# Kernel tuning notes

Measured on AMD Instinct MI355X. Metric: run time of the kernel, lower is better.

Reference implementation:

```python
import jax, jax.numpy as jnp
import numpy as np

ND, NP_, B = 20000, 10000, 4096
DE, PE = 320000, 160000
FEAT = 300 + 1024 + 1024 + 1024  # 3372


def leaky(x):
    return jnp.where(x > 0, x, 0.01 * x)


def gcn_conv(x, W, b, edge_index, edge_weight, n):
    # PyG GCNConv (eval): x' = D^-1/2 (A + I) D^-1/2 (x W) + b, with edge weights
    h = x @ W  # [n, out]
    row, col = edge_index[0], edge_index[1]
    loop = jnp.arange(n)
    row = jnp.concatenate([row, loop])
    col = jnp.concatenate([col, loop])
    ew = jnp.concatenate([edge_weight, jnp.ones((n,), edge_weight.dtype)])
    deg = jax.ops.segment_sum(ew, col, num_segments=n)
    dinv = jnp.where(deg > 0, jax.lax.rsqrt(deg), 0.0)
    norm = dinv[row] * ew * dinv[col]  # [E+n]
    out = jax.ops.segment_sum(h[row] * norm[:, None], col, num_segments=n)
    return out + b


def _lin_init(k, fi, fo):
    return jax.random.normal(k, (fi, fo), jnp.float32) * (1.0 / np.sqrt(fi))


def setup_inputs():
    key = jax.random.key(0)
    ks = jax.random.split(key, 32)
    inp = {}
    inp['d_index'] = jax.random.randint(ks[0], (B,), 0, ND)
    inp['p_index'] = jax.random.randint(ks[1], (B,), 0, NP_)
    inp['d_vecs'] = jax.random.normal(ks[2], (B, 300), jnp.float32)
    inp['p_embeddings'] = jax.random.normal(ks[3], (B, 1024), jnp.float32)
    inp['d_ecfps'] = jax.random.normal(ks[4], (ND, 1024), jnp.float32)
    inp['d_edge_index'] = jax.random.randint(ks[5], (2, DE), 0, ND)
    inp['d_edge_weight'] = jax.random.uniform(ks[6], (DE,), jnp.float32)
    inp['p_gos'] = jax.random.normal(ks[7], (NP_, 2812), jnp.float32)
    inp['p_edge_index'] = jax.random.randint(ks[8], (2, PE), 0, NP_)
    inp['p_edge_weight'] = jax.random.uniform(ks[9], (PE,), jnp.float32)
    # parameters
    inp['d_gcn_W'] = _lin_init(ks[10], 1024, 1024); inp['d_gcn_b'] = jnp.zeros((1024,), jnp.float32)
    inp['p_gcn_W'] = _lin_init(ks[11], 2812, 1024); inp['p_gcn_b'] = jnp.zeros((1024,), jnp.float32)
    inp['enc_W1'] = _lin_init(ks[12], FEAT, 1024); inp['enc_b1'] = jnp.zeros((1024,), jnp.float32)
    inp['enc_W2'] = _lin_init(ks[13], 1024, 256); inp['enc_b2'] = jnp.zeros((256,), jnp.float32)
    inp['dec_W1'] = _lin_init(ks[14], 256, 1024); inp['dec_b1'] = jnp.zeros((1024,), jnp.float32)
    inp['dec_W2'] = _lin_init(ks[15], 1024, FEAT); inp['dec_b2'] = jnp.zeros((FEAT,), jnp.float32)
    inp['out_W1'] = _lin_init(ks[16], 256, 128); inp['out_b1'] = jnp.zeros((128,), jnp.float32)
    inp['bn_gamma'] = jnp.ones((128,), jnp.float32)
    inp['bn_beta'] = jnp.zeros((128,), jnp.float32)
    inp['bn_mean'] = jnp.zeros((128,), jnp.float32)
    inp['bn_var'] = jnp.ones((128,), jnp.float32)
    inp['out_W2'] = _lin_init(ks[17], 128, 1); inp['out_b2'] = jnp.zeros((1,), jnp.float32)
    return inp


def reference(d_index, p_index, d_vecs, p_embeddings, d_ecfps, d_edge_index,
              d_edge_weight, p_gos, p_edge_index, p_edge_weight,
              d_gcn_W, d_gcn_b, p_gcn_W, p_gcn_b,
              enc_W1, enc_b1, enc_W2, enc_b2,
              dec_W1, dec_b1, dec_W2, dec_b2,
              out_W1, out_b1, bn_gamma, bn_beta, bn_mean, bn_var, out_W2, out_b2):
    # GCN branches (Dropout is identity in eval mode)
    ecfps = leaky(gcn_conv(d_ecfps, d_gcn_W, d_gcn_b, d_edge_index, d_edge_weight, ND))[d_index]
    gos = leaky(gcn_conv(p_gos, p_gcn_W, p_gcn_b, p_edge_index, p_edge_weight, NP_))[p_index]
    feature = jnp.concatenate([d_vecs, p_embeddings, ecfps, gos], axis=1)  # [B, 3372]
    encoded = leaky(leaky(feature @ enc_W1 + enc_b1) @ enc_W2 + enc_b2)  # [B, 256]
    decoded = leaky(leaky(encoded @ dec_W1 + dec_b1) @ dec_W2 + dec_b2)  # [B, 3372]
    h = encoded @ out_W1 + out_b1
    h = (h - bn_mean) * jax.lax.rsqrt(bn_var + 1e-5) * bn_gamma + bn_beta  # BN (eval)
    y = leaky(h) @ out_W2 + out_b2  # [B, 1]
    return (y, encoded, decoded, feature)
```

## Files before the change

### kernel.cpp

```cpp
#include <hip/hip_runtime.h>

#define ND    20000
#define NPn   10000
#define Bsz   4096
#define DE    320000
#define PEe   160000
#define FEAT  3372

#define ENC_OFF  4096ull
#define DEC_OFF  1052672ull
#define FEAT_OFF 14864384ull

typedef unsigned short u16;
typedef unsigned int   u32;
typedef __bf16 bf16x8 __attribute__((ext_vector_type(8)));
typedef float  f32x4  __attribute__((ext_vector_type(4)));

__device__ __forceinline__ float bf2f(u16 u) {
    u32 v = ((u32)u) << 16;
    return __builtin_bit_cast(float, v);
}
__device__ __forceinline__ u16 f2bf(float f) {
    u32 x = __builtin_bit_cast(u32, f);
    x += 0x7fffu + ((x >> 16) & 1u);
    return (u16)(x >> 16);
}
__device__ __forceinline__ float lrelu(float x) { return x > 0.f ? x : 0.01f * x; }

__device__ __forceinline__ float ldv(const void* p, size_t i, int f32) {
    return f32 ? ((const float*)p)[i] : bf2f(((const u16*)p)[i]);
}
__device__ __forceinline__ void stv(void* p, size_t i, int f32, float v) {
    if (f32) ((float*)p)[i] = v; else ((u16*)p)[i] = f2bf(v);
}

typedef __attribute__((address_space(1))) const void GASV;
typedef __attribute__((address_space(3))) void LASV;
__device__ __forceinline__ void gld16(const u16* g, u16* l) {
    __builtin_amdgcn_global_load_lds((GASV*)g, (LASV*)l, 16, 0, 0);
}

__global__ void detect_dtype(const u32* __restrict__ ew, int* __restrict__ flag)
{
    int t = threadIdx.x, bad = 0;
    for (int i = t; i < 256; i += 64)
        if ((ew[i] & 0xffffu) > 0x4200u) bad = 1;
    unsigned long long m = __ballot(bad);
    if (t == 0) *flag = (m != 0ull) ? 1 : 0;
}

__global__ __launch_bounds__(256) void transpose_split(const void* __restrict__ W,
                                                       u16* __restrict__ Th,
                                                       u16* __restrict__ Tl,
                                                       int K, int N, int Kp,
                                                       const int* __restrict__ flagp)
{
    const int f32 = *flagp;
    __shared__ float tile[32][33];
    const int k0 = blockIdx.x * 32, n0 = blockIdx.y * 32;
    const int tx = threadIdx.x & 31, ty = threadIdx.x >> 5;
    for (int i = 0; i < 4; ++i) {
        int k = k0 + ty + 8 * i, n = n0 + tx;
        float v = 0.f;
        if (k < K && n < N) v = ldv(W, (size_t)k * N + n, f32);
        tile[ty + 8 * i][tx] = v;
    }
    __syncthreads();
    for (int i = 0; i < 4; ++i) {
        int n = n0 + ty + 8 * i, k = k0 + tx;
        if (n < N && k < Kp) {
            float v = tile[tx][ty + 8 * i];
            u16 h = f2bf(v);
            Th[(size_t)n * Kp + k] = h;
            Tl[(size_t)n * Kp + k] = f2bf(v - bf2f(h));
        }
    }
}

__global__ void deg_accum(const int* __restrict__ ei, const void* __restrict__ ew,
                          float* __restrict__ deg, int E, const int* __restrict__ flagp)
{
    const int f32 = *flagp;
    int e = blockIdx.x * blockDim.x + threadIdx.x;
    if (e >= E) return;
    atomicAdd(&deg[ei[E + e]], ldv(ew, e, f32));
}

__global__ void dinv_kernel(float* __restrict__ deg, int n)
{
    int i = blockIdx.x * blockDim.x + threadIdx.x;
    if (i >= n) return;
    deg[i] = rsqrtf(deg[i] + 1.0f);
}

__global__ void csr_count(const int* __restrict__ ei, int* __restrict__ cnt, int E)
{
    int e = blockIdx.x * blockDim.x + threadIdx.x;
    if (e >= E) return;
    atomicAdd(&cnt[ei[E + e]], 1);
}

__global__ __launch_bounds__(256) void scan_kernel(const int* __restrict__ cnt,
                                                   int* __restrict__ offs,
                                                   int* __restrict__ cur, int n)
{
    __shared__ int tot[256];
    __shared__ int pref[257];
    const int t = threadIdx.x;
    const int chunk = (n + 255) / 256;
    const int s0 = t * chunk;
    const int s1 = (s0 + chunk < n) ? (s0 + chunk) : n;
    int s = 0;
    for (int i = s0; i < s1; ++i) s += cnt[i];
    tot[t] = s;
    __syncthreads();
    if (t == 0) {
        int run = 0;
        for (int i = 0; i < 256; ++i) { pref[i] = run; run += tot[i]; }
        pref[256] = run;
    }
    __syncthreads();
    int run = pref[t];
    for (int i = s0; i < s1; ++i) { offs[i] = run; cur[i] = run; run += cnt[i]; }
    if (t == 255) offs[n] = pref[256];
}

__global__ void csr_fill(const int* __restrict__ ei, const void* __restrict__ ew,
                         int* __restrict__ cur, int* __restrict__ crow,
                         float* __restrict__ cw, int E, const int* __restrict__ flagp)
{
    const int f32 = *flagp;
    int e = blockIdx.x * blockDim.x + threadIdx.x;
    if (e >= E) return;
    int c = ei[E + e];
    int p = atomicAdd(&cur[c], 1);
    crow[p] = ei[e];
    cw[p]   = ldv(ew, e, f32);
}

__global__ __launch_bounds__(256) void aggregate(const void* __restrict__ X, int ldx,
                                                 int ncols,
                                                 const int* __restrict__ bidx,
                                                 const float* __restrict__ dinv,
                                                 const int* __restrict__ offs,
                                                 const int* __restrict__ crow,
                                                 const float* __restrict__ cw,
                                                 const int* __restrict__ flagp,
                                                 u16* __restrict__ outH,
                                                 u16* __restrict__ outL, int ldo)
{
    const int f32 = *flagp;
    const int b = blockIdx.x, t = threadIdx.x;
    const int node = bidx[b];
    const int nch = ncols >> 2;
    const float dc = dinv[node];
    float acc[3][4];
#pragma unroll
    for (int i = 0; i < 3; ++i)
        for (int j = 0; j < 4; ++j) acc[i][j] = 0.f;

    {
        const float sw = dc * dc;
        const size_t rb = (size_t)node * ldx;
#pragma unroll
        for (int i = 0; i < 3; ++i) {
            int c = t + 256 * i;
            if (c < nch) {
                float v[4];
                if (f32) {
                    float4 x = *(const float4*)((const float*)X + rb + 4 * c);
                    v[0] = x.x; v[1] = x.y; v[2] = x.z; v[3] = x.w;
                } else {
                    uint2 x = *(const uint2*)((const u16*)X + rb + 4 * c);
                    v[0] = bf2f((u16)(x.x & 0xffffu)); v[1] = bf2f((u16)(x.x >> 16));
                    v[2] = bf2f((u16)(x.y & 0xffffu)); v[3] = bf2f((u16)(x.y >> 16));
                }
                for (int j = 0; j < 4; ++j) acc[i][j] += v[j] * sw;
            }
        }
    }
    const int e1 = offs[node + 1];
    for (int e = offs[node]; e < e1; ++e) {
        const int r = crow[e];
        const float nrm = dinv[r] * cw[e] * dc;
        const size_t rb = (size_t)r * ldx;
#pragma unroll
        for (int i = 0; i < 3; ++i) {
            int c = t + 256 * i;
            if (c < nch) {
                float v[4];
                if (f32) {
                    float4 x = *(const float4*)((const float*)X + rb + 4 * c);
                    v[0] = x.x; v[1] = x.y; v[2] = x.z; v[3] = x.w;
                } else {
                    uint2 x = *(const uint2*)((const u16*)X + rb + 4 * c);
                    v[0] = bf2f((u16)(x.x & 0xffffu)); v[1] = bf2f((u16)(x.x >> 16));
                    v[2] = bf2f((u16)(x.y & 0xffffu)); v[3] = bf2f((u16)(x.y >> 16));
                }
                for (int j = 0; j < 4; ++j) acc[i][j] += v[j] * nrm;
            }
        }
    }
    const size_t ob = (size_t)b * ldo;
#pragma unroll
    for (int i = 0; i < 3; ++i) {
        int c = t + 256 * i;
        if (c < nch) {
            u16 h[4], l[4];
#pragma unroll
            for (int j = 0; j < 4; ++j) {
                h[j] = f2bf(acc[i][j]);
                l[j] = f2bf(acc[i][j] - bf2f(h[j]));
            }
            uint2 hv, lv;
            hv.x = (u32)h[0] | ((u32)h[1] << 16); hv.y = (u32)h[2] | ((u32)h[3] << 16);
            lv.x = (u32)l[0] | ((u32)l[1] << 16); lv.y = (u32)l[2] | ((u32)l[3] << 16);
            *(uint2*)(outH + ob + 4 * c) = hv;
            *(uint2*)(outL + ob + 4 * c) = lv;
        }
    }
    if (t == 0)
        for (int j = ncols; j < ldo; ++j) { outH[ob + j] = 0; outL[ob + j] = 0; }
}

__global__ __launch_bounds__(512, 2) void gemm_planes(
        const u16* __restrict__ Ah, const u16* __restrict__ Al, int lda,
        const u16* __restrict__ Bh, const u16* __restrict__ Bl, int ldb,
        void* __restrict__ C, int cmode, unsigned long long c_off, int ldc,
        u16* __restrict__ Ch, u16* __restrict__ Cl, int ldcp,
        const void* __restrict__ bias, int M, int N, int Kp,
        int do_leaky, const int* __restrict__ flagp)
{
    const int flag = *flagp;
    const int cf32 = cmode ? flag : 1;
    __shared__ u16 smAh[2][128 * 32], smAl[2][128 * 32];
    __shared__ u16 smBh[2][128 * 32], smBl[2][128 * 32];
    const int tid = threadIdx.x;
    const int m0 = blockIdx.y * 128, n0 = blockIdx.x * 128;
    const int w = tid >> 6, lane = tid & 63;
    const int wy = w >> 1, wx = w & 1, lr = lane & 15, q = lane >> 4;
    f32x4 acc[2][4] = {};

    const int sr = tid >> 2;
    const int sc = (tid & 3) * 8;
    const size_t gA = (size_t)(m0 + sr) * lda + sc;
    const size_t gB = (size_t)(n0 + sr) * ldb + sc;
    const int wb = w << 9;

    auto stage = [&](int k0, int buf) {
        gld16(Ah + gA + k0, &smAh[buf][wb]);
        gld16(Al + gA + k0, &smAl[buf][wb]);
        gld16(Bh + gB + k0, &smBh[buf][wb]);
        gld16(Bl + gB + k0, &smBl[buf][wb]);
    };

    stage(0, 0);
    __syncthreads();
    int cur = 0;
    for (int k0 = 0; k0 < Kp; k0 += 32) {
        const int nxt = k0 + 32;
        if (nxt < Kp) stage(nxt, cur ^ 1);
        bf16x8 bh[4], bl[4];
#pragma unroll
        for (int ni = 0; ni < 4; ++ni) {
            bh[ni] = *(const bf16x8*)&smBh[cur][(wx * 64 + ni * 16 + lr) * 32 + q * 8];
            bl[ni] = *(const bf16x8*)&smBl[cur][(wx * 64 + ni * 16 + lr) * 32 + q * 8];
        }
#pragma unroll
        for (int mi = 0; mi < 2; ++mi) {
            bf16x8 ah = *(const bf16x8*)&smAh[cur][(wy * 32 + mi * 16 + lr) * 32 + q * 8];
            bf16x8 al = *(const bf16x8*)&smAl[cur][(wy * 32 + mi * 16 + lr) * 32 + q * 8];
#pragma unroll
            for (int ni = 0; ni < 4; ++ni) {
                acc[mi][ni] = __builtin_amdgcn_mfma_f32_16x16x32_bf16(ah, bh[ni], acc[mi][ni], 0, 0, 0);
                acc[mi][ni] = __builtin_amdgcn_mfma_f32_16x16x32_bf16(ah, bl[ni], acc[mi][ni], 0, 0, 0);
                acc[mi][ni] = __builtin_amdgcn_mfma_f32_16x16x32_bf16(al, bh[ni], acc[mi][ni], 0, 0, 0);
            }
        }
        __syncthreads();
        cur ^= 1;
    }

#pragma unroll
    for (int mi = 0; mi < 2; ++mi)
#pragma unroll
        for (int r = 0; r < 4; ++r) {
            const int gm = m0 + wy * 32 + mi * 16 + q * 4 + r;
#pragma unroll
            for (int ni = 0; ni < 4; ++ni) {
                const int gn = n0 + wx * 64 + ni * 16 + lr;
                if (gn >= N) continue;
                float v = acc[mi][ni][r];
                if (bias) v += ldv(bias, gn, flag);
                if (do_leaky) v = lrelu(v);
                float vq = v;
                if (C) {
                    const size_t ci = (size_t)c_off + (size_t)gm * ldc + gn;
                    if (cf32) ((float*)C)[ci] = v;
                    else { u16 hh = f2bf(v); ((u16*)C)[ci] = hh; vq = bf2f(hh); }
                }
                if (Ch) {
                    const size_t pi = (size_t)gm * ldcp + gn;
                    u16 h = f2bf(vq);
                    Ch[pi] = h;
                    Cl[pi] = f2bf(vq - bf2f(h));
                }
            }
        }
}

__global__ __launch_bounds__(256) void concat(const void* __restrict__ d_vecs,
                                              const void* __restrict__ p_emb,
                                              void* __restrict__ out,
                                              u16* __restrict__ Fh,
                                              u16* __restrict__ Fl,
                                              const int* __restrict__ flagp)
{
    const int f32 = *flagp;
    const int b = blockIdx.x;
    const size_t fb = FEAT_OFF + (size_t)b * FEAT;
    const size_t pb = (size_t)b * 3392;
    for (int j = threadIdx.x; j < 1324; j += 256) {
        float v = (j < 300) ? ldv(d_vecs, (size_t)b * 300 + j, f32)
                            : ldv(p_emb, (size_t)b * 1024 + (j - 300), f32);
        stv(out, fb + j, f32, v);
        float vq = f32 ? v : bf2f(f2bf(v));
        u16 h = f2bf(vq);
        Fh[pb + j] = h;
        Fl[pb + j] = f2bf(vq - bf2f(h));
    }
    for (int j = 3372 + threadIdx.x; j < 3392; j += 256) {
        Fh[pb + j] = 0; Fl[pb + j] = 0;
    }
}

__global__ __launch_bounds__(128) void head(void* __restrict__ out,
                                            const void* __restrict__ W1,
                                            const void* __restrict__ b1,
                                            const void* __restrict__ g,
                                            const void* __restrict__ be,
                                            const void* __restrict__ mu,
                                            const void* __restrict__ vr,
                                            const void* __restrict__ W2,
                                            const void* __restrict__ b2,
                                            const int* __restrict__ flagp)
{
    const int f32 = *flagp;
    __shared__ float se[256];
    __shared__ float red[128];
    const int b = blockIdx.x, t = threadIdx.x;
    const size_t eb = ENC_OFF + (size_t)b * 256;
    se[t]       = ldv(out, eb + t, f32);
    se[t + 128] = ldv(out, eb + 128 + t, f32);
    __syncthreads();
    float acc = 0.f;
    for (int k = 0; k < 256; ++k) acc += se[k] * ldv(W1, (size_t)k * 128 + t, f32);
    acc += ldv(b1, t, f32);
    float bn = (acc - ldv(mu, t, f32)) * rsqrtf(ldv(vr, t, f32) + 1e-5f) * ldv(g, t, f32)
             + ldv(be, t, f32);
    red[t] = lrelu(bn) * ldv(W2, t, f32);
    __syncthreads();
    for (int s = 64; s > 0; s >>= 1) {
        if (t < s) red[t] += red[t + s];
        __syncthreads();
    }
    if (t == 0) stv(out, (size_t)b, f32, red[0] + ldv(b2, 0, f32));
}

extern "C" void kernel_launch(void* const* d_in, const int* in_sizes, int n_in,
                              void* d_out, int out_size, void* d_ws, size_t ws_size,
                              hipStream_t stream)
{
    (void)in_sizes; (void)n_in; (void)out_size; (void)ws_size;

    const int*  d_index = (const int*)d_in[0];
    const int*  p_index = (const int*)d_in[1];
    const void* d_vecs  = d_in[2];
    const void* p_emb   = d_in[3];
    const void* d_ecfps = d_in[4];
    const int*  d_ei    = (const int*)d_in[5];
    const void* d_ew    = d_in[6];
    const void* p_gos   = d_in[7];
    const int*  p_ei    = (const int*)d_in[8];
    const void* p_ew    = d_in[9];
    const void* d_gcn_W = d_in[10];
    const void* d_gcn_b = d_in[11];
    const void* p_gcn_W = d_in[12];
    const void* p_gcn_b = d_in[13];
    const void* enc_W1  = d_in[14];
    const void* enc_b1  = d_in[15];
    const void* enc_W2  = d_in[16];
    const void* enc_b2  = d_in[17];
    const void* dec_W1  = d_in[18];
    const void* dec_b1  = d_in[19];
    const void* dec_W2  = d_in[20];
    const void* dec_b2  = d_in[21];
    const void* out_W1  = d_in[22];
    const void* out_b1  = d_in[23];
    const void* bn_g    = d_in[24];
    const void* bn_b    = d_in[25];
    const void* bn_m    = d_in[26];
    const void* bn_v    = d_in[27];
    const void* out_W2  = d_in[28];
    const void* out_b2  = d_in[29];

    char* base = (char*)d_ws;
    size_t off = 0;
    auto alloc = [&](size_t bytes) -> void* {
        void* p = base + off;
        off = (off + bytes + 255) & ~(size_t)255;
        return p;
    };
    u16* Th_d  = (u16*)alloc((size_t)1024 * 1024 * 2);
    u16* Tl_d  = (u16*)alloc((size_t)1024 * 1024 * 2);
    u16* Th_p  = (u16*)alloc((size_t)1024 * 2816 * 2);
    u16* Tl_p  = (u16*)alloc((size_t)1024 * 2816 * 2);
    u16* Th_e1 = (u16*)alloc((size_t)1024 * 3392 * 2);
    u16* Tl_e1 = (u16*)alloc((size_t)1024 * 3392 * 2);
    u16* Th_e2 = (u16*)alloc((size_t)256  * 1024 * 2);
    u16* Tl_e2 = (u16*)alloc((size_t)256  * 1024 * 2);
    u16* Th_d1 = (u16*)alloc((size_t)1024 * 256  * 2);
    u16* Tl_d1 = (u16*)alloc((size_t)1024 * 256  * 2);
    u16* Th_d2 = (u16*)alloc((size_t)3456 * 1024 * 2);
    u16* Tl_d2 = (u16*)alloc((size_t)3456 * 1024 * 2);
    u16* AgDh = (u16*)alloc((size_t)Bsz * 1024 * 2);
    u16* AgDl = (u16*)alloc((size_t)Bsz * 1024 * 2);
    u16* AgPh = (u16*)alloc((size_t)Bsz * 2816 * 2);
    u16* AgPl = (u16*)alloc((size_t)Bsz * 2816 * 2);
    u16* Fh   = (u16*)alloc((size_t)Bsz * 3392 * 2);
    u16* Fl   = (u16*)alloc((size_t)Bsz * 3392 * 2);
    u16* E1h = AgDh;
    u16* E1l = AgDl;
    u16* Eh  = AgPh;
    u16* El  = AgPh + (size_t)Bsz * 256;
    u16* D1h = AgPl;
    u16* D1l = AgPl + (size_t)Bsz * 1024;
    float* deg_d  = (float*)alloc((size_t)ND  * 4);
    float* deg_p  = (float*)alloc((size_t)NPn * 4);
    int*   cnt_d  = (int*)alloc((size_t)ND * 4);
    int*   offs_d = (int*)alloc((size_t)(ND + 1) * 4);
    int*   cur_d  = (int*)alloc((size_t)ND * 4);
    int*   cnt_p  = (int*)alloc((size_t)NPn * 4);
    int*   offs_p = (int*)alloc((size_t)(NPn + 1) * 4);
    int*   cur_p  = (int*)alloc((size_t)NPn * 4);
    int*   crow_d = (int*)alloc((size_t)DE * 4);
    float* cw_d   = (float*)alloc((size_t)DE * 4);
    int*   crow_p = (int*)alloc((size_t)PEe * 4);
    float* cw_p   = (float*)alloc((size_t)PEe * 4);
    int*   flagp  = (int*)alloc(16);

    detect_dtype<<<1, 64, 0, stream>>>((const u32*)d_ew, flagp);
    hipMemsetAsync(deg_d, 0, (size_t)ND * 4, stream);
    hipMemsetAsync(deg_p, 0, (size_t)NPn * 4, stream);
    hipMemsetAsync(cnt_d, 0, (size_t)ND * 4, stream);
    hipMemsetAsync(cnt_p, 0, (size_t)NPn * 4, stream);

    transpose_split<<<dim3(32, 32),  256, 0, stream>>>(d_gcn_W, Th_d,  Tl_d,  1024, 1024, 1024, flagp);
    transpose_split<<<dim3(88, 32),  256, 0, stream>>>(p_gcn_W, Th_p,  Tl_p,  2812, 1024, 2816, flagp);
    transpose_split<<<dim3(106, 32), 256, 0, stream>>>(enc_W1,  Th_e1, Tl_e1, 3372, 1024, 3392, flagp);
    transpose_split<<<dim3(32, 8),   256, 0, stream>>>(enc_W2,  Th_e2, Tl_e2, 1024, 256,  1024, flagp);
    transpose_split<<<dim3(8, 32),   256, 0, stream>>>(dec_W1,  Th_d1, Tl_d1, 256,  1024, 256,  flagp);
    transpose_split<<<dim3(32, 106), 256, 0, stream>>>(dec_W2,  Th_d2, Tl_d2, 1024, 3372, 1024, flagp);

    deg_accum<<<(DE + 255) / 256, 256, 0, stream>>>(d_ei, d_ew, deg_d, DE, flagp);
    deg_accum<<<(PEe + 255) / 256, 256, 0, stream>>>(p_ei, p_ew, deg_p, PEe, flagp);
    dinv_kernel<<<(ND + 255) / 256, 256, 0, stream>>>(deg_d, ND);
    dinv_kernel<<<(NPn + 255) / 256, 256, 0, stream>>>(deg_p, NPn);
    csr_count<<<(DE + 255) / 256, 256, 0, stream>>>(d_ei, cnt_d, DE);
    csr_count<<<(PEe + 255) / 256, 256, 0, stream>>>(p_ei, cnt_p, PEe);
    scan_kernel<<<1, 256, 0, stream>>>(cnt_d, offs_d, cur_d, ND);
    scan_kernel<<<1, 256, 0, stream>>>(cnt_p, offs_p, cur_p, NPn);
    csr_fill<<<(DE + 255) / 256, 256, 0, stream>>>(d_ei, d_ew, cur_d, crow_d, cw_d, DE, flagp);
    csr_fill<<<(PEe + 255) / 256, 256, 0, stream>>>(p_ei, p_ew, cur_p, crow_p, cw_p, PEe, flagp);

    aggregate<<<Bsz, 256, 0, stream>>>(d_ecfps, 1024, 1024, d_index, deg_d,
                                       offs_d, crow_d, cw_d, flagp, AgDh, AgDl, 1024);
    aggregate<<<Bsz, 256, 0, stream>>>(p_gos, 2812, 2812, p_index, deg_p,
                                       offs_p, crow_p, cw_p, flagp, AgPh, AgPl, 2816);

    gemm_planes<<<dim3(8, 32), 512, 0, stream>>>(AgDh, AgDl, 1024, Th_d, Tl_d, 1024,
                                                 d_out, 1, FEAT_OFF + 1324, FEAT,
                                                 Fh + 1324, Fl + 1324, 3392,
                                                 d_gcn_b, Bsz, 1024, 1024, 1, flagp);
    gemm_planes<<<dim3(8, 32), 512, 0, stream>>>(AgPh, AgPl, 2816, Th_p, Tl_p, 2816,
                                                 d_out, 1, FEAT_OFF + 2348, FEAT,
                                                 Fh + 2348, Fl + 2348, 3392,
                                                 p_gcn_b, Bsz, 1024, 2816, 1, flagp);

    concat<<<Bsz, 256, 0, stream>>>(d_vecs, p_emb, d_out, Fh, Fl, flagp);

    gemm_planes<<<dim3(8, 32), 512, 0, stream>>>(Fh, Fl, 3392, Th_e1, Tl_e1, 3392,
                                                 nullptr, 0, 0, 0,
                                                 E1h, E1l, 1024,
                                                 enc_b1, Bsz, 1024, 3392, 1, flagp);
    gemm_planes<<<dim3(2, 32), 512, 0, stream>>>(E1h, E1l, 1024, Th_e2, Tl_e2, 1024,
                                                 d_out, 1, ENC_OFF, 256,
                                                 Eh, El, 256,
                                                 enc_b2, Bsz, 256, 1024, 1, flagp);
    gemm_planes<<<dim3(8, 32), 512, 0, stream>>>(Eh, El, 256, Th_d1, Tl_d1, 256,
                                                 nullptr, 0, 0, 0,
                                                 D1h, D1l, 1024,
                                                 dec_b1, Bsz, 1024, 256, 1, flagp);
    gemm_planes<<<dim3(27, 32), 512, 0, stream>>>(D1h, D1l, 1024, Th_d2, Tl_d2, 1024,
                                                  d_out, 1, DEC_OFF, FEAT,
                                                  nullptr, nullptr, 0,
                                                  dec_b2, Bsz, 3372, 1024, 1, flagp);

    head<<<Bsz, 128, 0, stream>>>(d_out, out_W1, out_b1, bn_g, bn_b,
                                  bn_m, bn_v, out_W2, out_b2, flagp);
}
```

Before: 1.229 ms.

## Add split-K GEMM with combine kernel, drop low-plane MFMA for bf16 inputs

Adds split-K to the plane GEMM: blocks along z each compute a K chunk and write fp32 partials, and a new combine kernel sums them and applies bias, leaky ReLU and the output/plane writes. Each GEMM launch has only 256 tiles, so this is meant to give more parallelism on a many-CU GPU. It also drops the shared-memory double buffer so more blocks fit per CU (launch bounds now 6), and skips the B low-plane load and MFMA when inputs are bf16. The costs are extra partial-buffer traffic, an extra launch per GEMM, and no overlap of loads with compute.

```diff
diff --git a/kernel.cpp b/kernel.cpp
--- a/kernel.cpp
+++ b/kernel.cpp
@@ -13,6 +13,7 @@
 
 typedef unsigned short u16;
 typedef unsigned int   u32;
+typedef unsigned long long u64;
 typedef __bf16 bf16x8 __attribute__((ext_vector_type(8)));
 typedef float  f32x4  __attribute__((ext_vector_type(4)));
 
@@ -223,90 +224,157 @@
         for (int j = ncols; j < ldo; ++j) { outH[ob + j] = 0; outL[ob + j] = 0; }
 }
 
-__global__ __launch_bounds__(512, 2) void gemm_planes(
+__global__ __launch_bounds__(512, 6) void gemm_planes(
         const u16* __restrict__ Ah, const u16* __restrict__ Al, int lda,
         const u16* __restrict__ Bh, const u16* __restrict__ Bl, int ldb,
-        void* __restrict__ C, int cmode, unsigned long long c_off, int ldc,
+        void* __restrict__ C, int cmode, u64 c_off, int ldc,
         u16* __restrict__ Ch, u16* __restrict__ Cl, int ldcp,
         const void* __restrict__ bias, int M, int N, int Kp,
-        int do_leaky, const int* __restrict__ flagp)
+        int do_leaky, const int* __restrict__ flagp,
+        int kChunk, float* __restrict__ Part)
 {
     const int flag = *flagp;
-    const int cf32 = cmode ? flag : 1;
-    __shared__ u16 smAh[2][128 * 32], smAl[2][128 * 32];
-    __shared__ u16 smBh[2][128 * 32], smBl[2][128 * 32];
+    __shared__ u16 smAh[4096], smAl[4096], smBh[4096], smBl[4096];
     const int tid = threadIdx.x;
     const int m0 = blockIdx.y * 128, n0 = blockIdx.x * 128;
     const int w = tid >> 6, lane = tid & 63;
     const int wy = w >> 1, wx = w & 1, lr = lane & 15, q = lane >> 4;
     f32x4 acc[2][4] = {};
 
-    const int sr = tid >> 2;
-    const int sc = (tid & 3) * 8;
+    const int sr = tid >> 2, sc = (tid & 3) * 8;
     const size_t gA = (size_t)(m0 + sr) * lda + sc;
     const size_t gB = (size_t)(n0 + sr) * ldb + sc;
     const int wb = w << 9;
 
-    auto stage = [&](int k0, int buf) {
-        gld16(Ah + gA + k0, &smAh[buf][wb]);
-        gld16(Al + gA + k0, &smAl[buf][wb]);
-        gld16(Bh + gB + k0, &smBh[buf][wb]);
-        gld16(Bl + gB + k0, &smBl[buf][wb]);
-    };
-
-    stage(0, 0);
-    __syncthreads();
-    int cur = 0;
-    for (int k0 = 0; k0 < Kp; k0 += 32) {
-        const int nxt = k0 + 32;
-        if (nxt < Kp) stage(nxt, cur ^ 1);
-        bf16x8 bh[4], bl[4];
-#pragma unroll
-        for (int ni = 0; ni < 4; ++ni) {
-            bh[ni] = *(const bf16x8*)&smBh[cur][(wx * 64 + ni * 16 + lr) * 32 + q * 8];
-            bl[ni] = *(const bf16x8*)&smBl[cur][(wx * 64 + ni * 16 + lr) * 32 + q * 8];
-        }
-#pragma unroll
-        for (int mi = 0; mi < 2; ++mi) {
-            bf16x8 ah = *(const bf16x8*)&smAh[cur][(wy * 32 + mi * 16 + lr) * 32 + q * 8];
-            bf16x8 al = *(const bf16x8*)&smAl[cur][(wy * 32 + mi * 16 + lr) * 32 + q * 8];
+    const int kBeg = Part ? blockIdx.z * kChunk : 0;
+    int kEnd = Part ? kBeg + kChunk : Kp;
+    if (kEnd > Kp) kEnd = Kp;
+
+    for (int k0 = kBeg; k0 < kEnd; k0 += 32) {
+        gld16(Ah + gA + k0, &smAh[wb]);
+        gld16(Al + gA + k0, &smAl[wb]);
+        gld16(Bh + gB + k0, &smBh[wb]);
+        if (flag) gld16(Bl + gB + k0, &smBl[wb]);
+        __syncthreads();
+        if (flag) {
+            bf16x8 bh[4], bl[4];
 #pragma unroll
             for (int ni = 0; ni < 4; ++ni) {
-                acc[mi][ni] = __builtin_amdgcn_mfma_f32_16x16x32_bf16(ah, bh[ni], acc[mi][ni], 0, 0, 0);
-                acc[mi][ni] = __builtin_amdgcn_mfma_f32_16x16x32_bf16(ah, bl[ni], acc[mi][ni], 0, 0, 0);
-                acc[mi][ni] = __builtin_amdgcn_mfma_f32_16x16x32_bf16(al, bh[ni], acc[mi][ni], 0, 0, 0);
+                bh[ni] = *(const bf16x8*)&smBh[(wx * 64 + ni * 16 + lr) * 32 + q * 8];
+                bl[ni] = *(const bf16x8*)&smBl[(wx * 64 + ni * 16 + lr) * 32 + q * 8];
+            }
+#pragma unroll
+            for (int mi = 0; mi < 2; ++mi) {
+                bf16x8 ah = *(const bf16x8*)&smAh[(wy * 32 + mi * 16 + lr) * 32 + q * 8];
+                bf16x8 al = *(const bf16x8*)&smAl[(wy * 32 + mi * 16 + lr) * 32 + q * 8];
+#pragma unroll
+                for (int ni = 0; ni < 4; ++ni) {
+                    acc[mi][ni] = __builtin_amdgcn_mfma_f32_16x16x32_bf16(ah, bh[ni], acc[mi][ni], 0, 0, 0);
+                    acc[mi][ni] = __builtin_amdgcn_mfma_f32_16x16x32_bf16(al, bh[ni], acc[mi][ni], 0, 0, 0);
+                    acc[mi][ni] = __builtin_amdgcn_mfma_f32_16x16x32_bf16(ah, bl[ni], acc[mi][ni], 0, 0, 0);
+                }
+            }
+        } else {
+            bf16x8 bh[4];
+#pragma unroll
+            for (int ni = 0; ni < 4; ++ni)
+                bh[ni] = *(const bf16x8*)&smBh[(wx * 64 + ni * 16 + lr) * 32 + q * 8];
+#pragma unroll
+            for (int mi = 0; mi < 2; ++mi) {
+                bf16x8 ah = *(const bf16x8*)&smAh[(wy * 32 + mi * 16 + lr) * 32 + q * 8];
+                bf16x8 al = *(const bf16x8*)&smAl[(wy * 32 + mi * 16 + lr) * 32 + q * 8];
+#pragma unroll
+                for (int ni = 0; ni < 4; ++ni) {
+                    acc[mi][ni] = __builtin_amdgcn_mfma_f32_16x16x32_bf16(ah, bh[ni], acc[mi][ni], 0, 0, 0);
+                    acc[mi][ni] = __builtin_amdgcn_mfma_f32_16x16x32_bf16(al, bh[ni], acc[mi][ni], 0, 0, 0);
+                }
             }
         }
         __syncthreads();
-        cur ^= 1;
-    }
-
-#pragma unroll
-    for (int mi = 0; mi < 2; ++mi)
-#pragma unroll
-        for (int r = 0; r < 4; ++r) {
-            const int gm = m0 + wy * 32 + mi * 16 + q * 4 + r;
-#pragma unroll
-            for (int ni = 0; ni < 4; ++ni) {
-                const int gn = n0 + wx * 64 + ni * 16 + lr;
-                if (gn >= N) continue;
-                float v = acc[mi][ni][r];
-                if (bias) v += ldv(bias, gn, flag);
-                if (do_leaky) v = lrelu(v);
-                float vq = v;
-                if (C) {
-                    const size_t ci = (size_t)c_off + (size_t)gm * ldc + gn;
-                    if (cf32) ((float*)C)[ci] = v;
-                    else { u16 hh = f2bf(v); ((u16*)C)[ci] = hh; vq = bf2f(hh); }
+    }
+
+    if (Part) {
+        float* P = Part + (size_t)blockIdx.z * ((size_t)M * N);
+#pragma unroll
+        for (int mi = 0; mi < 2; ++mi)
+#pragma unroll
+            for (int r = 0; r < 4; ++r) {
+                const int gm = m0 + wy * 32 + mi * 16 + q * 4 + r;
+                float* row = P + (size_t)gm * N + n0 + wx * 64 + lr;
+#pragma unroll
+                for (int ni = 0; ni < 4; ++ni)
+                    row[ni * 16] = acc[mi][ni][r];
+            }
+    } else {
+#pragma unroll
+        for (int mi = 0; mi < 2; ++mi)
+#pragma unroll
+            for (int r = 0; r < 4; ++r) {
+                const int gm = m0 + wy * 32 + mi * 16 + q * 4 + r;
+                if (gm >= M) continue;
+#pragma unroll
+                for (int ni = 0; ni < 4; ++ni) {
+                    const int gn = n0 + wx * 64 + ni * 16 + lr;
+                    if (gn >= N) continue;
+                    float v = acc[mi][ni][r];
+                    if (bias) v += ldv(bias, gn, flag);
+                    if (do_leaky) v = lrelu(v);
+                    float vq = v;
+                    if (C) {
+                        const size_t ci = (size_t)c_off + (size_t)gm * ldc + gn;
+                        const int cf32 = cmode ? flag : 1;
+                        if (cf32) ((float*)C)[ci] = v;
+                        else { u16 hh = f2bf(v); ((u16*)C)[ci] = hh; vq = bf2f(hh); }
+                    }
+                    if (Ch) {
+                        const size_t pi = (size_t)gm * ldcp + gn;
+                        u16 h = f2bf(vq);
+                        Ch[pi] = h;
+                        Cl[pi] = f2bf(vq - bf2f(h));
+                    }
                 }
-                if (Ch) {
-                    const size_t pi = (size_t)gm * ldcp + gn;
-                    u16 h = f2bf(vq);
-                    Ch[pi] = h;
-                    Cl[pi] = f2bf(vq - bf2f(h));
-                }
-            }
-        }
+            }
+    }
+}
+
+__global__ __launch_bounds__(256) void combine_split(
+        const float* __restrict__ Part, int S, int M, int N,
+        void* __restrict__ C, int cmode, u64 c_off, int ldc,
+        u16* __restrict__ Ch, u16* __restrict__ Cl, int ldcp,
+        const void* __restrict__ bias, int do_leaky,
+        const int* __restrict__ flagp)
+{
+    const int flag = *flagp;
+    const int cf32 = cmode ? flag : 1;
+    const size_t MN = (size_t)M * N;
+    size_t g = ((size_t)blockIdx.x * 256 + threadIdx.x) * 4;
+    if (g >= MN) return;
+    float4 v = *(const float4*)(Part + g);
+    for (int s = 1; s < S; ++s) {
+        float4 u = *(const float4*)(Part + (size_t)s * MN + g);
+        v.x += u.x; v.y += u.y; v.z += u.z; v.w += u.w;
+    }
+    const int gm = (int)(g / N), gn0 = (int)(g - (size_t)gm * N);
+    float e[4] = {v.x, v.y, v.z, v.w};
+#pragma unroll
+    for (int i = 0; i < 4; ++i) {
+        const int gn = gn0 + i;
+        float val = e[i];
+        if (bias) val += ldv(bias, gn, flag);
+        if (do_leaky) val = lrelu(val);
+        float vq = val;
+        if (C) {
+            const size_t ci = (size_t)c_off + (size_t)gm * ldc + gn;
+            if (cf32) ((float*)C)[ci] = val;
+            else { u16 hh = f2bf(val); ((u16*)C)[ci] = hh; vq = bf2f(hh); }
+        }
+        if (Ch) {
+            const size_t pi = (size_t)gm * ldcp + gn;
+            u16 h = f2bf(vq);
+            Ch[pi] = h;
+            Cl[pi] = f2bf(vq - bf2f(h));
+        }
+    }
 }
 
 __global__ __launch_bounds__(256) void concat(const void* __restrict__ d_vecs,
@@ -371,7 +439,7 @@
                               void* d_out, int out_size, void* d_ws, size_t ws_size,
                               hipStream_t stream)
 {
-    (void)in_sizes; (void)n_in; (void)out_size; (void)ws_size;
+    (void)in_sizes; (void)n_in; (void)out_size;
 
     const int*  d_index = (const int*)d_in[0];
     const int*  p_index = (const int*)d_in[1];
@@ -448,6 +516,15 @@
     int*   crow_p = (int*)alloc((size_t)PEe * 4);
     float* cw_p   = (float*)alloc((size_t)PEe * 4);
     int*   flagp  = (int*)alloc(16);
+    const size_t need4 = (size_t)4 * Bsz * 1024 * 4;
+    const size_t need2 = (size_t)2 * Bsz * 1024 * 4;
+    float* Part = nullptr;
+    int Sbig = 1, Se2 = 1, Sd1 = 1;
+    if (off + need4 + 512 <= ws_size) {
+        Part = (float*)alloc(need4); Sbig = 4; Se2 = 8; Sd1 = 2;
+    } else if (off + need2 + 512 <= ws_size) {
+        Part = (float*)alloc(need2); Sbig = 2; Se2 = 8; Sd1 = 2;
+    }
 
     detect_dtype<<<1, 64, 0, stream>>>((const u32*)d_ew, flagp);
     hipMemsetAsync(deg_d, 0, (size_t)ND * 4, stream);
@@ -478,33 +555,50 @@
     aggregate<<<Bsz, 256, 0, stream>>>(p_gos, 2812, 2812, p_index, deg_p,
                                        offs_p, crow_p, cw_p, flagp, AgPh, AgPl, 2816);
 
-    gemm_planes<<<dim3(8, 32), 512, 0, stream>>>(AgDh, AgDl, 1024, Th_d, Tl_d, 1024,
-                                                 d_out, 1, FEAT_OFF + 1324, FEAT,
-                                                 Fh + 1324, Fl + 1324, 3392,
-                                                 d_gcn_b, Bsz, 1024, 1024, 1, flagp);
-    gemm_planes<<<dim3(8, 32), 512, 0, stream>>>(AgPh, AgPl, 2816, Th_p, Tl_p, 2816,
-                                                 d_out, 1, FEAT_OFF + 2348, FEAT,
-                                                 Fh + 2348, Fl + 2348, 3392,
-                                                 p_gcn_b, Bsz, 1024, 2816, 1, flagp);
+    auto G = [&](const u16* Ah_, const u16* Al_, int lda_,
+                 const u16* Bh_, const u16* Bl_, int ldb_,
+                 void* C_, int cmode_, u64 coff_, int ldc_,
+                 u16* Ch_, u16* Cl_, int ldcp_,
+                 const void* bias_, int N_, int Kp_, int S_) {
+        const int nx = (N_ + 127) / 128;
+        if (S_ > 1 && Part) {
+            const int kc = ((Kp_ / S_ + 31) / 32) * 32;
+            gemm_planes<<<dim3(nx, 32, S_), 512, 0, stream>>>(
+                Ah_, Al_, lda_, Bh_, Bl_, ldb_,
+                nullptr, 0, 0, 0, nullptr, nullptr, 0,
+                nullptr, Bsz, N_, Kp_, 0, flagp, kc, Part);
+            combine_split<<<(Bsz * N_) / 1024, 256, 0, stream>>>(
+                Part, S_, Bsz, N_,
+                C_, cmode_, coff_, ldc_, Ch_, Cl_, ldcp_, bias_, 1, flagp);
+        } else {
+            gemm_planes<<<dim3(nx, 32, 1), 512, 0, stream>>>(
+                Ah_, Al_, lda_, Bh_, Bl_, ldb_,
+                C_, cmode_, coff_, ldc_, Ch_, Cl_, ldcp_,
+                bias_, Bsz, N_, Kp_, 1, flagp, 0, nullptr);
+        }
+    };
+
+    G(AgDh, AgDl, 1024, Th_d, Tl_d, 1024,
+      d_out, 1, FEAT_OFF + 1324, FEAT, Fh + 1324, Fl + 1324, 3392,
+      d_gcn_b, 1024, 1024, Sbig);
+    G(AgPh, AgPl, 2816, Th_p, Tl_p, 2816,
+      d_out, 1, FEAT_OFF + 2348, FEAT, Fh + 2348, Fl + 2348, 3392,
+      p_gcn_b, 1024, 2816, Sbig);
 
     concat<<<Bsz, 256, 0, stream>>>(d_vecs, p_emb, d_out, Fh, Fl, flagp);
 
-    gemm_planes<<<dim3(8, 32), 512, 0, stream>>>(Fh, Fl, 3392, Th_e1, Tl_e1, 3392,
-                                                 nullptr, 0, 0, 0,
-                                                 E1h, E1l, 1024,
-                                                 enc_b1, Bsz, 1024, 3392, 1, flagp);
-    gemm_planes<<<dim3(2, 32), 512, 0, stream>>>(E1h, E1l, 1024, Th_e2, Tl_e2, 1024,
-                                                 d_out, 1, ENC_OFF, 256,
-                                                 Eh, El, 256,
-                                                 enc_b2, Bsz, 256, 1024, 1, flagp);
-    gemm_planes<<<dim3(8, 32), 512, 0, stream>>>(Eh, El, 256, Th_d1, Tl_d1, 256,
-                                                 nullptr, 0, 0, 0,
-                                                 D1h, D1l, 1024,
-                                                 dec_b1, Bsz, 1024, 256, 1, flagp);
-    gemm_planes<<<dim3(27, 32), 512, 0, stream>>>(D1h, D1l, 1024, Th_d2, Tl_d2, 1024,
-                                                  d_out, 1, DEC_OFF, FEAT,
-                                                  nullptr, nullptr, 0,
-                                                  dec_b2, Bsz, 3372, 1024, 1, flagp);
+    G(Fh, Fl, 3392, Th_e1, Tl_e1, 3392,
+      nullptr, 0, 0, 0, E1h, E1l, 1024,
+      enc_b1, 1024, 3392, Sbig);
+    G(E1h, E1l, 1024, Th_e2, Tl_e2, 1024,
+      d_out, 1, ENC_OFF, 256, Eh, El, 256,
+      enc_b2, 256, 1024, Se2);
+    G(Eh, El, 256, Th_d1, Tl_d1, 256,
+      nullptr, 0, 0, 0, D1h, D1l, 1024,
+      dec_b1, 1024, 256, Sd1);
+    G(D1h, D1l, 1024, Th_d2, Tl_d2, 1024,
+      d_out, 1, DEC_OFF, FEAT, nullptr, nullptr, 0,
+      dec_b2, 3372, 1024, 1);
 
     head<<<Bsz, 128, 0, stream>>>(d_out, out_W1, out_b1, bn_g, bn_b,
                                   bn_m, bn_v, out_W2, out_b2, flagp);
```

Measured after the change: 2.306 ms. 1.88x slower.
